# Performance work log

Hardware: AMD Instinct MI355X
Metric: run time of the kernel (lower is better)

Reference implementation:

```python
import jax, jax.numpy as jnp
import numpy as np

TOPK = 8  # n_activated_experts


def setup_inputs() -> dict:
    key = jax.random.key(0)
    k1, k2 = jax.random.split(key)
    tokens, dim, n_experts = 8192, 4096, 64
    x = jax.random.normal(k1, (tokens, dim), dtype=jnp.float32)
    weight = jax.random.normal(k2, (n_experts, dim), dtype=jnp.float32) * 0.02
    bias = jnp.zeros((n_experts,), dtype=jnp.float32)
    return {"x": x, "weight": weight, "bias": bias}


def reference(x, weight, bias):
    # scores: [tokens, n_experts]
    scores = jnp.einsum("td,ed->te", x, weight) + bias
    probs = jax.nn.softmax(scores, axis=-1)  # score_func == 'softmax'
    weights, indices = jax.lax.top_k(probs, TOPK)
    return probs, indices
```

## Files before the change

### kernel.cpp

```cpp
#include <hip/hip_runtime.h>
#include <math.h>

#define NTOK    8192
#define DIM     4096
#define NEXP    64
#define TOPK_N  8
#define TAU     2.0e-4f
#define KSPLIT  8
#define KSTEPS  ((DIM / KSPLIT) / 32)

#define WS_WHI_OFF  0
#define WS_WLO_OFF  524288

typedef __attribute__((ext_vector_type(8))) short short8;
typedef __attribute__((ext_vector_type(4))) float f32x4;

__device__ __forceinline__ void cvt8(float4 a0, float4 a1, short8& hv, short8& lv) {
    float f[8] = {a0.x, a0.y, a0.z, a0.w, a1.x, a1.y, a1.z, a1.w};
    union { short8 v; unsigned u[4]; } H, L;
    #pragma unroll
    for (int i = 0; i < 4; ++i) {
        unsigned b0 = __float_as_uint(f[2*i]);
        unsigned b1 = __float_as_uint(f[2*i+1]);
        float r0 = f[2*i]   - __uint_as_float(b0 & 0xffff0000u);
        float r1 = f[2*i+1] - __uint_as_float(b1 & 0xffff0000u);
        H.u[i] = (b0 >> 16) | (b1 & 0xffff0000u);
        L.u[i] = (__float_as_uint(r0) >> 16) | (__float_as_uint(r1) & 0xffff0000u);
    }
    hv = H.v; lv = L.v;
}

__global__ __launch_bounds__(256, 4)
void cvt_w_kernel(const float* __restrict__ w, unsigned short* __restrict__ whi,
                  unsigned short* __restrict__ wlo) {
    const int g = blockIdx.x * 256 + threadIdx.x;
    const float* p = w + (size_t)g * 16;
    union { short8 v; uint4 q; } H[2], L[2];
    #pragma unroll
    for (int h = 0; h < 2; ++h) {
        float4 a0 = *(const float4*)(p + h * 8);
        float4 a1 = *(const float4*)(p + h * 8 + 4);
        cvt8(a0, a1, H[h].v, L[h].v);
    }
    *(uint4*)(whi + (size_t)g * 16)     = H[0].q;
    *(uint4*)(whi + (size_t)g * 16 + 8) = H[1].q;
    *(uint4*)(wlo + (size_t)g * 16)     = L[0].q;
    *(uint4*)(wlo + (size_t)g * 16 + 8) = L[1].q;
}

__global__ __launch_bounds__(512, 2)
void gemm_kernel(const float* __restrict__ x, const unsigned short* __restrict__ whi,
                 const unsigned short* __restrict__ wlo, const float* __restrict__ bias,
                 const float* __restrict__ wfp, float* __restrict__ out, int ntok) {
    __shared__ float  lds_part[KSPLIT][32][65];
    __shared__ float  lds_s[32][65];
    __shared__ double dsc[NEXP];
    __shared__ int    nflag;
    __shared__ int    ftok[32];
    __shared__ float  fninth[32];

    const int tid  = threadIdx.x;
    const int lane = tid & 63;
    const int wv   = tid >> 6;
    const int nl   = lane & 15;
    const int q    = lane >> 4;
    const int tok0 = blockIdx.x * 32;
    if (tid == 0) nflag = 0;

    const int kbase = wv * (DIM / KSPLIT);
    const float* xr[2] = { x + (size_t)(tok0 + nl) * DIM,
                           x + (size_t)(tok0 + 16 + nl) * DIM };
    size_t boff[4];
    #pragma unroll
    for (int nf = 0; nf < 4; ++nf) boff[nf] = (size_t)(nf * 16 + nl) * DIM;

    f32x4 acc[2][4];
    #pragma unroll
    for (int mg = 0; mg < 2; ++mg)
        #pragma unroll
        for (int nf = 0; nf < 4; ++nf) acc[mg][nf] = (f32x4){0.f, 0.f, 0.f, 0.f};

    float4 Ar[2][2][2];
    short8 Bh[2][4], Bl[2][4];

    {
        const int k0 = kbase + q * 8;
        #pragma unroll
        for (int mg = 0; mg < 2; ++mg) {
            Ar[0][mg][0] = *(const float4*)(xr[mg] + k0);
            Ar[0][mg][1] = *(const float4*)(xr[mg] + k0 + 4);
        }
        #pragma unroll
        for (int nf = 0; nf < 4; ++nf) {
            Bh[0][nf] = *(const short8*)(whi + boff[nf] + k0);
            Bl[0][nf] = *(const short8*)(wlo + boff[nf] + k0);
        }
    }

    #pragma unroll 2
    for (int ks = 0; ks < KSTEPS; ++ks) {
        const int buf = ks & 1, nxt = buf ^ 1;
        if (ks + 1 < KSTEPS) {
            const int k1 = kbase + (ks + 1) * 32 + q * 8;
            #pragma unroll
            for (int mg = 0; mg < 2; ++mg) {
                Ar[nxt][mg][0] = *(const float4*)(xr[mg] + k1);
                Ar[nxt][mg][1] = *(const float4*)(xr[mg] + k1 + 4);
            }
            #pragma unroll
            for (int nf = 0; nf < 4; ++nf) {
                Bh[nxt][nf] = *(const short8*)(whi + boff[nf] + k1);
                Bl[nxt][nf] = *(const short8*)(wlo + boff[nf] + k1);
            }
        }
        short8 ahi[2], alo[2];
        cvt8(Ar[buf][0][0], Ar[buf][0][1], ahi[0], alo[0]);
        cvt8(Ar[buf][1][0], Ar[buf][1][1], ahi[1], alo[1]);
        #pragma unroll
        for (int mg = 0; mg < 2; ++mg)
            #pragma unroll
            for (int nf = 0; nf < 4; ++nf) {
                acc[mg][nf] = __builtin_amdgcn_mfma_f32_16x16x32_bf16(ahi[mg], Bl[buf][nf], acc[mg][nf], 0, 0, 0);
                acc[mg][nf] = __builtin_amdgcn_mfma_f32_16x16x32_bf16(alo[mg], Bh[buf][nf], acc[mg][nf], 0, 0, 0);
                acc[mg][nf] = __builtin_amdgcn_mfma_f32_16x16x32_bf16(ahi[mg], Bh[buf][nf], acc[mg][nf], 0, 0, 0);
            }
    }

    #pragma unroll
    for (int mg = 0; mg < 2; ++mg)
        #pragma unroll
        for (int nf = 0; nf < 4; ++nf)
            #pragma unroll
            for (int r = 0; r < 4; ++r)
                lds_part[wv][mg * 16 + q * 4 + r][nf * 16 + nl] = acc[mg][nf][r];
    __syncthreads();

    #pragma unroll
    for (int i = 0; i < 4; ++i) {
        const int p  = tid + i * 512;
        const int tk = p >> 6, e = p & 63;
        float s = lds_part[0][tk][e];
        #pragma unroll
        for (int k = 1; k < KSPLIT; ++k) s += lds_part[k][tk][e];
        lds_s[tk][e] = s + bias[e];
    }
    __syncthreads();

    float* __restrict__ out_idx = out + (size_t)ntok * NEXP;
    #pragma unroll
    for (int t = 0; t < 4; ++t) {
        const int tokl = wv * 4 + t;
        const int tok  = tok0 + tokl;
        const float s  = lds_s[tokl][lane];

        float m = s;
        #pragma unroll
        for (int off = 32; off > 0; off >>= 1)
            m = fmaxf(m, __shfl_xor(m, off, 64));
        const float ex = expf(s - m);
        float sum = ex;
        #pragma unroll
        for (int off = 32; off > 0; off >>= 1)
            sum += __shfl_xor(sum, off, 64);
        out[(size_t)tok * NEXP + lane] = ex / sum;

        float cv = s, prev = 0.f, ming = 1e30f;
        for (int r = 0; r < TOPK_N + 1; ++r) {
            float bv = cv;
            int   bi = lane;
            #pragma unroll
            for (int off = 32; off > 0; off >>= 1) {
                const float ov = __shfl_xor(bv, off, 64);
                const int   oi = __shfl_xor(bi, off, 64);
                if (ov > bv || (ov == bv && oi < bi)) { bv = ov; bi = oi; }
            }
            if (r > 0) ming = fminf(ming, prev - bv);
            prev = bv;
            if (r < TOPK_N && lane == r)
                out_idx[(size_t)tok * TOPK_N + r] = (float)bi;
            if (lane == bi) cv = -INFINITY;
        }
        if (lane == 0 && ming < TAU) {
            const int sl = atomicAdd(&nflag, 1);
            ftok[sl] = tokl;
            fninth[sl] = prev;
        }
    }
    __syncthreads();

    const int nfl = nflag;
    for (int i = 0; i < nfl; ++i) {
        const int tokl = ftok[i];
        const int tok  = tok0 + tokl;
        const float thr = fninth[i] - TAU;
        const unsigned long long cmask = __ballot(lds_s[tokl][lane] >= thr);
        if (wv == 0) dsc[lane] = -1.0e300;
        __syncthreads();
        {
            int rank = 0;
            unsigned long long mm = cmask;
            while (mm) {
                const int e = __builtin_ctzll(mm);
                mm &= mm - 1;
                if ((rank & 7) == wv) {
                    const float* wr = wfp + (size_t)e * DIM;
                    const float* xrr = x + (size_t)tok * DIM;
                    double a = 0.0;
                    #pragma unroll 4
                    for (int kk = 0; kk < 16; ++kk) {
                        const int k = kk * 256 + lane * 4;
                        const float4 wv4 = *(const float4*)(wr + k);
                        const float4 xv  = *(const float4*)(xrr + k);
                        a = fma((double)xv.x, (double)wv4.x, a);
                        a = fma((double)xv.y, (double)wv4.y, a);
                        a = fma((double)xv.z, (double)wv4.z, a);
                        a = fma((double)xv.w, (double)wv4.w, a);
                    }
                    #pragma unroll
                    for (int off = 32; off > 0; off >>= 1)
                        a += __shfl_xor(a, off, 64);
                    if (lane == 0) dsc[e] = a + (double)bias[e];
                }
                ++rank;
            }
        }
        __syncthreads();
        if (wv == 0) {
            double cv = dsc[lane];
            for (int r = 0; r < TOPK_N; ++r) {
                double bv = cv;
                int    bi = lane;
                #pragma unroll
                for (int off = 32; off > 0; off >>= 1) {
                    const double ov = __shfl_xor(bv, off, 64);
                    const int    oi = __shfl_xor(bi, off, 64);
                    if (ov > bv || (ov == bv && oi < bi)) { bv = ov; bi = oi; }
                }
                if (lane == r)
                    out_idx[(size_t)tok * TOPK_N + r] = (float)bi;
                if (lane == bi) cv = -1.0e301;
            }
        }
        __syncthreads();
    }
}

extern "C" void kernel_launch(void* const* d_in, const int* in_sizes, int n_in,
                              void* d_out, int out_size, void* d_ws, size_t ws_size,
                              hipStream_t stream) {
    const float* x  = (const float*)d_in[0];
    const float* w  = (const float*)d_in[1];
    const float* bs = (const float*)d_in[2];
    float* out = (float*)d_out;

    unsigned short* whi = (unsigned short*)((char*)d_ws + WS_WHI_OFF);
    unsigned short* wlo = (unsigned short*)((char*)d_ws + WS_WLO_OFF);

    const int ntok = in_sizes[0] / DIM;

    hipLaunchKernelGGL(cvt_w_kernel, dim3((NEXP * DIM) / 16 / 256), dim3(256), 0, stream,
                       w, whi, wlo);
    hipLaunchKernelGGL(gemm_kernel, dim3(ntok / 32), dim3(512), 0, stream,
                       x, whi, wlo, bs, w, out, ntok);
}
```

Before: 256.0 us.

## Halve token tile per block and replace iterative top-k with rank counting

Each GEMM block now handles 16 tokens instead of 32, giving twice as many blocks and a higher occupancy target (launch bounds 512,4) for better latency hiding. The nine-round shuffle-argmax top-k becomes a parallel rank computation in which each lane counts larger scores from LDS, and the near-tie check is moved to a per-token pass over a small top9 buffer. The weight conversion kernel uses 8 elements per thread. The cost is that each block reloads the full bf16 weight split, doubling weight traffic through L2, and has less reuse per B load.

New measurement: 264.6 us. 3.4% more time.

```diff
diff --git a/kernel.cpp b/kernel.cpp
--- a/kernel.cpp
+++ b/kernel.cpp
@@ -8,6 +8,7 @@
 #define TAU     2.0e-4f
 #define KSPLIT  8
 #define KSTEPS  ((DIM / KSPLIT) / 32)
+#define TB      16
 
 #define WS_WHI_OFF  0
 #define WS_WLO_OFF  524288
@@ -34,62 +35,52 @@
 void cvt_w_kernel(const float* __restrict__ w, unsigned short* __restrict__ whi,
                   unsigned short* __restrict__ wlo) {
     const int g = blockIdx.x * 256 + threadIdx.x;
-    const float* p = w + (size_t)g * 16;
-    union { short8 v; uint4 q; } H[2], L[2];
-    #pragma unroll
-    for (int h = 0; h < 2; ++h) {
-        float4 a0 = *(const float4*)(p + h * 8);
-        float4 a1 = *(const float4*)(p + h * 8 + 4);
-        cvt8(a0, a1, H[h].v, L[h].v);
-    }
-    *(uint4*)(whi + (size_t)g * 16)     = H[0].q;
-    *(uint4*)(whi + (size_t)g * 16 + 8) = H[1].q;
-    *(uint4*)(wlo + (size_t)g * 16)     = L[0].q;
-    *(uint4*)(wlo + (size_t)g * 16 + 8) = L[1].q;
-}
-
-__global__ __launch_bounds__(512, 2)
+    const float* p = w + (size_t)g * 8;
+    union { short8 v; uint4 q; } H, L;
+    float4 a0 = *(const float4*)(p);
+    float4 a1 = *(const float4*)(p + 4);
+    cvt8(a0, a1, H.v, L.v);
+    *(uint4*)(whi + (size_t)g * 8) = H.q;
+    *(uint4*)(wlo + (size_t)g * 8) = L.q;
+}
+
+__global__ __launch_bounds__(512, 4)
 void gemm_kernel(const float* __restrict__ x, const unsigned short* __restrict__ whi,
                  const unsigned short* __restrict__ wlo, const float* __restrict__ bias,
                  const float* __restrict__ wfp, float* __restrict__ out, int ntok) {
-    __shared__ float  lds_part[KSPLIT][32][65];
-    __shared__ float  lds_s[32][65];
+    __shared__ float  lds_part[KSPLIT][TB][65];
+    __shared__ float  lds_s[TB][68];
+    __shared__ float  top9[TB][9];
     __shared__ double dsc[NEXP];
     __shared__ int    nflag;
-    __shared__ int    ftok[32];
-    __shared__ float  fninth[32];
+    __shared__ int    ftok[TB];
+    __shared__ float  fninth[TB];
 
     const int tid  = threadIdx.x;
     const int lane = tid & 63;
     const int wv   = tid >> 6;
     const int nl   = lane & 15;
     const int q    = lane >> 4;
-    const int tok0 = blockIdx.x * 32;
+    const int tok0 = blockIdx.x * TB;
     if (tid == 0) nflag = 0;
 
     const int kbase = wv * (DIM / KSPLIT);
-    const float* xr[2] = { x + (size_t)(tok0 + nl) * DIM,
-                           x + (size_t)(tok0 + 16 + nl) * DIM };
+    const float* xr = x + (size_t)(tok0 + nl) * DIM;
     size_t boff[4];
     #pragma unroll
     for (int nf = 0; nf < 4; ++nf) boff[nf] = (size_t)(nf * 16 + nl) * DIM;
 
-    f32x4 acc[2][4];
-    #pragma unroll
-    for (int mg = 0; mg < 2; ++mg)
-        #pragma unroll
-        for (int nf = 0; nf < 4; ++nf) acc[mg][nf] = (f32x4){0.f, 0.f, 0.f, 0.f};
-
-    float4 Ar[2][2][2];
+    f32x4 acc[4];
+    #pragma unroll
+    for (int nf = 0; nf < 4; ++nf) acc[nf] = (f32x4){0.f, 0.f, 0.f, 0.f};
+
+    float4 Ar[2][2];
     short8 Bh[2][4], Bl[2][4];
 
     {
         const int k0 = kbase + q * 8;
-        #pragma unroll
-        for (int mg = 0; mg < 2; ++mg) {
-            Ar[0][mg][0] = *(const float4*)(xr[mg] + k0);
-            Ar[0][mg][1] = *(const float4*)(xr[mg] + k0 + 4);
-        }
+        Ar[0][0] = *(const float4*)(xr + k0);
+        Ar[0][1] = *(const float4*)(xr + k0 + 4);
         #pragma unroll
         for (int nf = 0; nf < 4; ++nf) {
             Bh[0][nf] = *(const short8*)(whi + boff[nf] + k0);
@@ -102,41 +93,33 @@
         const int buf = ks & 1, nxt = buf ^ 1;
         if (ks + 1 < KSTEPS) {
             const int k1 = kbase + (ks + 1) * 32 + q * 8;
-            #pragma unroll
-            for (int mg = 0; mg < 2; ++mg) {
-                Ar[nxt][mg][0] = *(const float4*)(xr[mg] + k1);
-                Ar[nxt][mg][1] = *(const float4*)(xr[mg] + k1 + 4);
-            }
+            Ar[nxt][0] = *(const float4*)(xr + k1);
+            Ar[nxt][1] = *(const float4*)(xr + k1 + 4);
             #pragma unroll
             for (int nf = 0; nf < 4; ++nf) {
                 Bh[nxt][nf] = *(const short8*)(whi + boff[nf] + k1);
                 Bl[nxt][nf] = *(const short8*)(wlo + boff[nf] + k1);
             }
         }
-        short8 ahi[2], alo[2];
-        cvt8(Ar[buf][0][0], Ar[buf][0][1], ahi[0], alo[0]);
-        cvt8(Ar[buf][1][0], Ar[buf][1][1], ahi[1], alo[1]);
-        #pragma unroll
-        for (int mg = 0; mg < 2; ++mg)
-            #pragma unroll
-            for (int nf = 0; nf < 4; ++nf) {
-                acc[mg][nf] = __builtin_amdgcn_mfma_f32_16x16x32_bf16(ahi[mg], Bl[buf][nf], acc[mg][nf], 0, 0, 0);
-                acc[mg][nf] = __builtin_amdgcn_mfma_f32_16x16x32_bf16(alo[mg], Bh[buf][nf], acc[mg][nf], 0, 0, 0);
-                acc[mg][nf] = __builtin_amdgcn_mfma_f32_16x16x32_bf16(ahi[mg], Bh[buf][nf], acc[mg][nf], 0, 0, 0);
-            }
-    }
-
-    #pragma unroll
-    for (int mg = 0; mg < 2; ++mg)
-        #pragma unroll
-        for (int nf = 0; nf < 4; ++nf)
-            #pragma unroll
-            for (int r = 0; r < 4; ++r)
-                lds_part[wv][mg * 16 + q * 4 + r][nf * 16 + nl] = acc[mg][nf][r];
-    __syncthreads();
-
-    #pragma unroll
-    for (int i = 0; i < 4; ++i) {
+        short8 ahi, alo;
+        cvt8(Ar[buf][0], Ar[buf][1], ahi, alo);
+        #pragma unroll
+        for (int nf = 0; nf < 4; ++nf) {
+            acc[nf] = __builtin_amdgcn_mfma_f32_16x16x32_bf16(ahi, Bl[buf][nf], acc[nf], 0, 0, 0);
+            acc[nf] = __builtin_amdgcn_mfma_f32_16x16x32_bf16(alo, Bh[buf][nf], acc[nf], 0, 0, 0);
+            acc[nf] = __builtin_amdgcn_mfma_f32_16x16x32_bf16(ahi, Bh[buf][nf], acc[nf], 0, 0, 0);
+        }
+    }
+
+    #pragma unroll
+    for (int nf = 0; nf < 4; ++nf)
+        #pragma unroll
+        for (int r = 0; r < 4; ++r)
+            lds_part[wv][q * 4 + r][nf * 16 + nl] = acc[nf][r];
+    __syncthreads();
+
+    #pragma unroll
+    for (int i = 0; i < (TB * NEXP) / 512; ++i) {
         const int p  = tid + i * 512;
         const int tk = p >> 6, e = p & 63;
         float s = lds_part[0][tk][e];
@@ -148,8 +131,8 @@
 
     float* __restrict__ out_idx = out + (size_t)ntok * NEXP;
     #pragma unroll
-    for (int t = 0; t < 4; ++t) {
-        const int tokl = wv * 4 + t;
+    for (int t = 0; t < 2; ++t) {
+        const int tokl = wv * 2 + t;
         const int tok  = tok0 + tokl;
         const float s  = lds_s[tokl][lane];
 
@@ -164,26 +147,30 @@
             sum += __shfl_xor(sum, off, 64);
         out[(size_t)tok * NEXP + lane] = ex / sum;
 
-        float cv = s, prev = 0.f, ming = 1e30f;
-        for (int r = 0; r < TOPK_N + 1; ++r) {
-            float bv = cv;
-            int   bi = lane;
-            #pragma unroll
-            for (int off = 32; off > 0; off >>= 1) {
-                const float ov = __shfl_xor(bv, off, 64);
-                const int   oi = __shfl_xor(bi, off, 64);
-                if (ov > bv || (ov == bv && oi < bi)) { bv = ov; bi = oi; }
-            }
-            if (r > 0) ming = fminf(ming, prev - bv);
-            prev = bv;
-            if (r < TOPK_N && lane == r)
-                out_idx[(size_t)tok * TOPK_N + r] = (float)bi;
-            if (lane == bi) cv = -INFINITY;
-        }
-        if (lane == 0 && ming < TAU) {
+        int rank = 0;
+        #pragma unroll
+        for (int i = 0; i < 16; ++i) {
+            const float4 v4 = *(const float4*)(&lds_s[tokl][i * 4]);
+            rank += (int)((v4.x > s) || (v4.x == s && (i * 4 + 0) < lane));
+            rank += (int)((v4.y > s) || (v4.y == s && (i * 4 + 1) < lane));
+            rank += (int)((v4.z > s) || (v4.z == s && (i * 4 + 2) < lane));
+            rank += (int)((v4.w > s) || (v4.w == s && (i * 4 + 3) < lane));
+        }
+        if (rank < TOPK_N + 1) top9[tokl][rank] = s;
+        if (rank < TOPK_N)
+            out_idx[(size_t)tok * TOPK_N + rank] = (float)lane;
+    }
+    __syncthreads();
+
+    if (tid < TB) {
+        float ming = 1e30f;
+        #pragma unroll
+        for (int r = 0; r < TOPK_N; ++r)
+            ming = fminf(ming, top9[tid][r] - top9[tid][r + 1]);
+        if (ming < TAU) {
             const int sl = atomicAdd(&nflag, 1);
-            ftok[sl] = tokl;
-            fninth[sl] = prev;
+            ftok[sl] = tid;
+            fninth[sl] = top9[tid][TOPK_N];
         }
     }
     __syncthreads();
@@ -203,7 +190,7 @@
                 const int e = __builtin_ctzll(mm);
                 mm &= mm - 1;
                 if ((rank & 7) == wv) {
-                    const float* wr = wfp + (size_t)e * DIM;
+                    const float* wr  = wfp + (size_t)e * DIM;
                     const float* xrr = x + (size_t)tok * DIM;
                     double a = 0.0;
                     #pragma unroll 4
@@ -258,8 +245,8 @@
 
     const int ntok = in_sizes[0] / DIM;
 
-    hipLaunchKernelGGL(cvt_w_kernel, dim3((NEXP * DIM) / 16 / 256), dim3(256), 0, stream,
+    hipLaunchKernelGGL(cvt_w_kernel, dim3((NEXP * DIM) / 8 / 256), dim3(256), 0, stream,
                        w, whi, wlo);
-    hipLaunchKernelGGL(gemm_kernel, dim3(ntok / 32), dim3(512), 0, stream,
+    hipLaunchKernelGGL(gemm_kernel, dim3(ntok / TB), dim3(512), 0, stream,
                        x, whi, wlo, bs, w, out, ntok);
 }
```
